# Performance work log

Hardware: AMD Instinct MI355X
Metric: run time of the kernel (lower is better)

Reference implementation:

```python
import jax, jax.numpy as jnp
import numpy as np

B = 256        # graphs per batch (python loop in original, vectorized here)
N = 512        # nodes per graph
DEG = 16       # avg degree
E_PER = N * DEG
T = 64         # num_node_types
D = 128        # gnn_hidden_dim


def setup_inputs() -> dict:
    key = jax.random.key(0)
    ks = jax.random.split(key, 8)
    node_feat = jax.random.randint(ks[0], (B * N,), 0, T)
    offs = (jnp.arange(B) * N)[:, None]
    src = (jax.random.randint(ks[1], (B, E_PER), 0, N) + offs).reshape(-1)
    dst = (jax.random.randint(ks[2], (B, E_PER), 0, N) + offs).reshape(-1)
    emb_table = jax.random.normal(ks[3], (T, D), dtype=jnp.float32) * 0.02
    W1 = jax.random.normal(ks[4], (D, D), dtype=jnp.float32) * (1.0 / np.sqrt(D))
    b1 = jnp.zeros((D,), dtype=jnp.float32)
    W2 = jax.random.normal(ks[5], (D, D), dtype=jnp.float32) * (1.0 / np.sqrt(D))
    b2 = jnp.zeros((D,), dtype=jnp.float32)
    return {"node_feat": node_feat, "src": src, "dst": dst,
            "emb_table": emb_table, "W1": W1, "b1": b1, "W2": W2, "b2": b2}


def _gcn_layer(h, src, dst, out_isqrt, in_isqrt, W, b, n):
    # DGL GraphConv, norm='both': D_in^{-1/2} A D_out^{-1/2} h W + b
    m = (h * out_isqrt[:, None])[src]                      # [E, D] gather
    agg = jax.ops.segment_sum(m, dst, num_segments=n)      # [Ntot, D] scatter
    return (agg * in_isqrt[:, None]) @ W + b


def reference(node_feat, src, dst, emb_table, W1, b1, W2, b2):
    n = node_feat.shape[0]
    ones = jnp.ones(src.shape[0], dtype=emb_table.dtype)
    deg_out = jnp.clip(jax.ops.segment_sum(ones, src, num_segments=n), 1.0)
    deg_in = jnp.clip(jax.ops.segment_sum(ones, dst, num_segments=n), 1.0)
    out_isqrt = jax.lax.rsqrt(deg_out)
    in_isqrt = jax.lax.rsqrt(deg_in)

    h = emb_table[node_feat]                                # [Ntot, D]
    # layer 1 (dropout is eval-mode identity) + relu, layer 2 + relu
    h = jax.nn.relu(_gcn_layer(h, src, dst, out_isqrt, in_isqrt, W1, b1, n))
    h = jax.nn.relu(_gcn_layer(h, src, dst, out_isqrt, in_isqrt, W2, b2, n))

    # dgl.mean_nodes per graph, then mean_gnn_embeddings + stack -> [B, D]
    gid = jnp.arange(n) // N
    hg = jax.ops.segment_sum(h, gid, num_segments=B) / float(N)
    return hg
```

## Files before the change

### kernel.cpp

```cpp
#include <hip/hip_runtime.h>
#include <stdint.h>

#define GRAPHS 256
#define NPG    512
#define EPG    8192

typedef __attribute__((ext_vector_type(8))) short s16x8;
typedef __attribute__((ext_vector_type(4))) float f32x4;

__device__ __forceinline__ float bf2f(unsigned short u){
  union { unsigned int i; float f; } c; c.i = ((unsigned int)u)<<16; return c.f;
}
__device__ __forceinline__ unsigned short f2bf(float f){
  union { float f; unsigned int i; } c; c.f = f;
  unsigned int r = c.i + 0x7fffu + ((c.i>>16)&1u);
  return (unsigned short)(r>>16);
}

__global__ __launch_bounds__(128) void k_prep(const float* __restrict__ emb,
      const float* __restrict__ W1, const float* __restrict__ W2,
      unsigned short* __restrict__ EW1T, unsigned short* __restrict__ W2F){
  const int b = blockIdx.x, tid = threadIdx.x;
  if (tid < 32){
    const int gid = b*32 + tid;
    const int t = gid>>7, c = gid&127;
    float acc=0.f;
    #pragma unroll 4
    for (int k=0;k<128;k++) acc += emb[t*128+k]*W1[k*128+c];
    EW1T[c*64+t]=f2bf(acc);
  } else if (tid >= 64){
    const int i = b*64 + (tid-64);
    const int ks = i>>12, nt=(i>>9)&7, ln=(i>>3)&63, j=i&7;
    const int k = ks*32 + (ln>>4)*8 + j;
    const int n = nt*16 + (ln&15);
    W2F[i] = f2bf(W2[k*128+n]);
  }
}

#define OFF_SORT 0
#define OFF_CS   16384
#define OFF_WSC  18440
#define OFF_WINT 20488
#define OFF_B1   22536
#define OFF_B2   23048
#define OFF_H1F  23568
#define OFF_SINT 89104
#define OFF_CSRA 23568
#define OFF_A    23568
#define OFF_ABF  40464
#define OFF_GBH  73744
#define OFF_GBL  82448
#define FUSED_LDS 158736

__global__ __launch_bounds__(512,2) void k_fused(
      const int* __restrict__ src, const int* __restrict__ dst,
      const int* __restrict__ ntype, const float* __restrict__ b1,
      const float* __restrict__ b2, const unsigned short* __restrict__ EW1T,
      const unsigned short* __restrict__ W2F, float* __restrict__ out){
  extern __shared__ char smem[];
  unsigned short* sorted16 = (unsigned short*)(smem + OFF_SORT);
  int*   cs   = (int*)(smem + OFF_CS);
  float* wsc  = (float*)(smem + OFF_WSC);
  int*   wint = (int*)(smem + OFF_WINT);
  float* b1sh = (float*)(smem + OFF_B1);
  float* b2sh = (float*)(smem + OFF_B2);
  unsigned short* h1F = (unsigned short*)(smem + OFF_H1F);
  int*   Sint = (int*)(smem + OFF_SINT);
  unsigned char*  A   = (unsigned char*)(smem + OFF_A);
  unsigned int*   A32 = (unsigned int*)(smem + OFF_A);
  unsigned short* Abf = (unsigned short*)(smem + OFF_ABF);
  unsigned short* gbh = (unsigned short*)(smem + OFF_GBH);
  unsigned short* gbl = (unsigned short*)(smem + OFF_GBL);
  float* red = (float*)(smem + OFF_A);
  int* hist   = (int*)(smem + OFF_CSRA);
  int* cursor = hist + 512;
  int* co     = cursor + 512;
  unsigned short* ntype_sh = (unsigned short*)(co + 512);

  const int b = blockIdx.x, tid = threadIdx.x;
  const int eb = b*EPG, nb = b*NPG;

  hist[tid]=0; co[tid]=0; ntype_sh[tid]=(unsigned short)ntype[nb+tid];
  if (tid<128){ b1sh[tid]=b1[tid]; b2sh[tid]=b2[tid]; }
  __syncthreads();
  int4 d4[4], s4[4];
  {
    const int4* dv = (const int4*)(dst+eb);
    const int4* sv = (const int4*)(src+eb);
    #pragma unroll
    for (int j=0;j<4;j++){
      d4[j]=dv[tid + j*512];
      s4[j]=sv[tid + j*512];
      atomicAdd(&hist[d4[j].x&(NPG-1)],1); atomicAdd(&hist[d4[j].y&(NPG-1)],1);
      atomicAdd(&hist[d4[j].z&(NPG-1)],1); atomicAdd(&hist[d4[j].w&(NPG-1)],1);
      atomicAdd(&co[s4[j].x&(NPG-1)],1);   atomicAdd(&co[s4[j].y&(NPG-1)],1);
      atomicAdd(&co[s4[j].z&(NPG-1)],1);   atomicAdd(&co[s4[j].w&(NPG-1)],1);
    }
  }
  __syncthreads();
  if (tid<64){
    int carry=0;
    #pragma unroll
    for (int c=0;c<8;c++){
      int sc=hist[64*c+tid];
      #pragma unroll
      for (int off=1;off<64;off<<=1){ int y=__shfl_up(sc,off); if (tid>=off) sc+=y; }
      cs[64*c+tid+1]=carry+sc;
      carry+=__shfl(sc,63);
    }
    if (tid==0) cs[0]=0;
  }
  __syncthreads();
  cursor[tid]=cs[tid];
  __syncthreads();
  #pragma unroll
  for (int j=0;j<4;j++){
    int dl, s, pos;
    dl=d4[j].x&(NPG-1); s=s4[j].x&(NPG-1);
    pos=atomicAdd(&cursor[dl],1);
    sorted16[pos]=(unsigned short)(((unsigned int)ntype_sh[s]<<9)|(unsigned int)s);
    dl=d4[j].y&(NPG-1); s=s4[j].y&(NPG-1);
    pos=atomicAdd(&cursor[dl],1);
    sorted16[pos]=(unsigned short)(((unsigned int)ntype_sh[s]<<9)|(unsigned int)s);
    dl=d4[j].z&(NPG-1); s=s4[j].z&(NPG-1);
    pos=atomicAdd(&cursor[dl],1);
    sorted16[pos]=(unsigned short)(((unsigned int)ntype_sh[s]<<9)|(unsigned int)s);
    dl=d4[j].w&(NPG-1); s=s4[j].w&(NPG-1);
    pos=atomicAdd(&cursor[dl],1);
    sorted16[pos]=(unsigned short)(((unsigned int)ntype_sh[s]<<9)|(unsigned int)s);
  }
  {
    int a=co[tid]; if(a<1)a=1;
    const float w = rsqrtf((float)a);
    wsc[tid]=w; wint[tid]=(int)(w*1048576.f);
  }
  __syncthreads();

  const int wave=tid>>6, lane=tid&63, l16=lane&15, quad=lane>>4;

  #pragma unroll 1
  for (int h=0; h<2; ++h){
    const int v0 = h*256;
    for (int i=tid; i<(256*68)/4; i+=512) ((f32x4*)Sint)[i]=(f32x4){0.f,0.f,0.f,0.f};
    __syncthreads();
    {
      const int r = tid>>1, p = tid&1;
      const int e1 = cs[v0+r+1];
      for (int i=cs[v0+r]+p; i<e1; i+=2){
        const unsigned int e = sorted16[i];
        atomicAdd(&Sint[r*68 + (int)(e>>9)], wint[e&511]);
      }
    }
    __syncthreads();
    f32x4 acc1[2][8];
    #pragma unroll
    for (int rt=0;rt<2;rt++)
      #pragma unroll
      for (int nt=0;nt<8;nt++) acc1[rt][nt]=(f32x4){0.f,0.f,0.f,0.f};
    #pragma unroll
    for (int kh=0; kh<2; ++kh){
      s16x8 fh[2], fl[2];
      #pragma unroll
      for (int rt=0;rt<2;rt++){
        const int m = (wave*2+rt)*16 + l16;
        const int* sp = &Sint[m*68 + kh*32 + quad*8];
        union { s16x8 v; unsigned short u[8]; } hv, lv;
        #pragma unroll
        for (int j=0;j<8;j++){
          const float f = (float)sp[j] * (1.f/1048576.f);
          const unsigned short hi = f2bf(f);
          hv.u[j]=hi; lv.u[j]=f2bf(f - bf2f(hi));
        }
        fh[rt]=hv.v; fl[rt]=lv.v;
      }
      const int kc = kh*32 + quad*8;
      #pragma unroll
      for (int nt=0;nt<8;nt++){
        s16x8 bfr=__builtin_bit_cast(s16x8,
            *(const uint4*)(EW1T + (size_t)(nt*16+l16)*64 + kc));
        acc1[0][nt]=__builtin_amdgcn_mfma_f32_16x16x32_bf16(fh[0],bfr,acc1[0][nt],0,0,0);
        acc1[1][nt]=__builtin_amdgcn_mfma_f32_16x16x32_bf16(fh[1],bfr,acc1[1][nt],0,0,0);
        acc1[0][nt]=__builtin_amdgcn_mfma_f32_16x16x32_bf16(fl[0],bfr,acc1[0][nt],0,0,0);
        acc1[1][nt]=__builtin_amdgcn_mfma_f32_16x16x32_bf16(fl[1],bfr,acc1[1][nt],0,0,0);
      }
    }
    float isq[2][4], os[2][4];
    #pragma unroll
    for (int rt=0;rt<2;rt++){
      const int mloc = (wave*2+rt)*16 + quad*4;
      #pragma unroll
      for (int r=0;r<4;r++){
        int d = cs[v0+mloc+r+1]-cs[v0+mloc+r]; if (d<1) d=1;
        isq[rt][r]=rsqrtf((float)d);
        os[rt][r]=wsc[v0+mloc+r];
      }
    }
    __syncthreads();
    #pragma unroll
    for (int rt=0;rt<2;rt++){
      const int ksg = h*8 + wave;
      const int kq  = rt*2 + (quad>>1);
      const int j0  = (quad&1)*4;
      #pragma unroll
      for (int nt=0;nt<8;nt++){
        const int col = nt*16+l16;
        const float bb1 = b1sh[col];
        ushort4 st;
        st.x = f2bf(fmaxf(acc1[rt][nt][0]*isq[rt][0]+bb1,0.f)*os[rt][0]);
        st.y = f2bf(fmaxf(acc1[rt][nt][1]*isq[rt][1]+bb1,0.f)*os[rt][1]);
        st.z = f2bf(fmaxf(acc1[rt][nt][2]*isq[rt][2]+bb1,0.f)*os[rt][2]);
        st.w = f2bf(fmaxf(acc1[rt][nt][3]*isq[rt][3]+bb1,0.f)*os[rt][3]);
        *(ushort4*)(h1F + ((((ksg*8+nt)*64) + kq*16 + l16)*8 + j0)) = st;
      }
    }
    __syncthreads();
  }

  s16x8 bh[16];
  #pragma unroll
  for (int ks=0;ks<16;ks++)
    bh[ks] = __builtin_bit_cast(s16x8,
        *(const uint4*)(h1F + (((ks*8+wave)*64 + lane)*8)));
  uint4 w2q[4];
  #pragma unroll
  for (int ks2=0;ks2<4;ks2++)
    w2q[ks2] = *(const uint4*)(W2F + (size_t)(((ks2*8+wave)*64)+lane)*8);
  const float bb2 = b2sh[wave*16+l16];
  __syncthreads();
  for (int i=tid; i<16896/16; i+=512) ((uint4*)A)[i]=(uint4){0u,0u,0u,0u};
  __syncthreads();
  float pp = 0.f;
  const int crow = tid>>4, ccol = (tid&15)*32;

  #pragma unroll 1
  for (int dt=0; dt<16; ++dt){
    const int r0 = dt*32;
    {
      const int r = tid>>4, p = tid&15;
      const int e1 = cs[r0+r+1];
      for (int i=cs[r0+r]+p; i<e1; i+=16){
        const int s = (int)(sorted16[i] & 511u);
        atomicAdd(&A32[r*132 + (s>>2)], 1u<<((s&3)*8));
      }
    }
    __syncthreads();
    {
      unsigned char* ap = A + crow*528 + ccol;
      const uint4 w0c = *(const uint4*)ap;
      const uint4 w1c = *(const uint4*)(ap+16);
      *(uint4*)ap = (uint4){0u,0u,0u,0u};
      *(uint4*)(ap+16) = (uint4){0u,0u,0u,0u};
      unsigned int wd[8] = {w0c.x,w0c.y,w0c.z,w0c.w,w1c.x,w1c.y,w1c.z,w1c.w};
      const int gb = (ccol>>3), sw = crow&7;
      #pragma unroll
      for (int ch=0; ch<4; ++ch){
        uint4 st;
        unsigned int u0=wd[2*ch], u1=wd[2*ch+1];
        {
          const float g0=(float)( u0       &0xffu);
          const float g1=(float)((u0>> 8u) &0xffu);
          const float g2=(float)((u0>>16u) &0xffu);
          const float g3=(float)( u0>>24u        );
          st.x=__builtin_amdgcn_perm(__builtin_bit_cast(unsigned int,g1),
                                     __builtin_bit_cast(unsigned int,g0),0x07060302u);
          st.y=__builtin_amdgcn_perm(__builtin_bit_cast(unsigned int,g3),
                                     __builtin_bit_cast(unsigned int,g2),0x07060302u);
        }
        {
          const float g0=(float)( u1       &0xffu);
          const float g1=(float)((u1>> 8u) &0xffu);
          const float g2=(float)((u1>>16u) &0xffu);
          const float g3=(float)( u1>>24u        );
          st.z=__builtin_amdgcn_perm(__builtin_bit_cast(unsigned int,g1),
                                     __builtin_bit_cast(unsigned int,g0),0x07060302u);
          st.w=__builtin_amdgcn_perm(__builtin_bit_cast(unsigned int,g3),
                                     __builtin_bit_cast(unsigned int,g2),0x07060302u);
        }
        *(uint4*)(Abf + crow*520 + (((gb+ch)^sw)<<3)) = st;
      }
    }
    __syncthreads();
    f32x4 g0=(f32x4){0.f,0.f,0.f,0.f}, g1=(f32x4){0.f,0.f,0.f,0.f};
    #pragma unroll
    for (int ks=0;ks<16;ks++){
      const int gsw = ((ks*4+quad) ^ (l16&7))<<3;
      const s16x8 a0 = __builtin_bit_cast(s16x8,
          *(const uint4*)(Abf + ( 0+l16)*520 + gsw));
      const s16x8 a1 = __builtin_bit_cast(s16x8,
          *(const uint4*)(Abf + (16+l16)*520 + gsw));
      g0=__builtin_amdgcn_mfma_f32_16x16x32_bf16(a0, bh[ks], g0,0,0,0);
      g1=__builtin_amdgcn_mfma_f32_16x16x32_bf16(a1, bh[ks], g1,0,0,0);
    }
    #pragma unroll
    for (int ri=0;ri<4;ri++){
      {
        const int row = quad*4+ri;
        int d = cs[r0+row+1]-cs[r0+row]; if (d<1) d=1;
        const float gs = g0[ri]*rsqrtf((float)d);
        const unsigned short hi = f2bf(gs);
        gbh[row*136 + wave*16+l16] = hi;
        gbl[row*136 + wave*16+l16] = f2bf(gs - bf2f(hi));
      }
      {
        const int row = 16+quad*4+ri;
        int d = cs[r0+row+1]-cs[r0+row]; if (d<1) d=1;
        const float gs = g1[ri]*rsqrtf((float)d);
        const unsigned short hi = f2bf(gs);
        gbh[row*136 + wave*16+l16] = hi;
        gbl[row*136 + wave*16+l16] = f2bf(gs - bf2f(hi));
      }
    }
    __syncthreads();
    f32x4 h30=(f32x4){0.f,0.f,0.f,0.f}, h31=(f32x4){0.f,0.f,0.f,0.f};
    #pragma unroll
    for (int ks2=0;ks2<4;ks2++){
      const int ko = ks2*32 + quad*8;
      h30=__builtin_amdgcn_mfma_f32_16x16x32_bf16(__builtin_bit_cast(s16x8,
          *(const uint4*)(gbh + ( 0+l16)*136 + ko)),
          __builtin_bit_cast(s16x8,w2q[ks2]), h30,0,0,0);
      h30=__builtin_amdgcn_mfma_f32_16x16x32_bf16(__builtin_bit_cast(s16x8,
          *(const uint4*)(gbl + ( 0+l16)*136 + ko)),
          __builtin_bit_cast(s16x8,w2q[ks2]), h30,0,0,0);
      h31=__builtin_amdgcn_mfma_f32_16x16x32_bf16(__builtin_bit_cast(s16x8,
          *(const uint4*)(gbh + (16+l16)*136 + ko)),
          __builtin_bit_cast(s16x8,w2q[ks2]), h31,0,0,0);
      h31=__builtin_amdgcn_mfma_f32_16x16x32_bf16(__builtin_bit_cast(s16x8,
          *(const uint4*)(gbl + (16+l16)*136 + ko)),
          __builtin_bit_cast(s16x8,w2q[ks2]), h31,0,0,0);
    }
    #pragma unroll
    for (int ri=0;ri<4;ri++){
      pp += fmaxf(h30[ri]+bb2, 0.f);
      pp += fmaxf(h31[ri]+bb2, 0.f);
    }
  }

  pp += __shfl_xor(pp,16);
  pp += __shfl_xor(pp,32);
  __syncthreads();
  if (quad==0) red[wave*16+l16] = pp;
  __syncthreads();
  if (tid<128) out[(size_t)b*128 + tid] = red[tid]*(1.f/512.f);
}

extern "C" void kernel_launch(void* const* d_in, const int* in_sizes, int n_in,
                              void* d_out, int out_size, void* d_ws, size_t ws_size,
                              hipStream_t stream){
  const int* node_feat = (const int*)d_in[0];
  const int* src = (const int*)d_in[1];
  const int* dst = (const int*)d_in[2];
  const float* emb = (const float*)d_in[3];
  const float* W1  = (const float*)d_in[4];
  const float* b1  = (const float*)d_in[5];
  const float* W2  = (const float*)d_in[6];
  const float* b2  = (const float*)d_in[7];

  char* ws = (char*)d_ws;
  unsigned short* EW1T = (unsigned short*)(ws);
  unsigned short* W2F  = (unsigned short*)(ws + 16384);

  (void)hipFuncSetAttribute(reinterpret_cast<const void*>(&k_fused),
        hipFuncAttributeMaxDynamicSharedMemorySize, FUSED_LDS);

  k_prep<<<GRAPHS,128,0,stream>>>(emb,W1,W2,EW1T,W2F);
  k_fused<<<GRAPHS,512,FUSED_LDS,stream>>>(src,dst,node_feat,b1,b2,EW1T,W2F,
        (float*)d_out);
}
```

Baseline: 166.4 us.

## Double threads per graph block to 1024 and split MFMA tiles across 16 waves

The fused per-graph kernel moves from 512 to 1024 threads per block. Edge loading, the weighted scatter, and the adjacency build are spread over more threads, and each of the 16 waves now computes one 16-row MFMA tile instead of two, with a final reduction over the two row halves. The prep kernel is also regridded to 64 blocks of 512 threads, and the layer-1 dot product is split over two lanes joined with a shuffle. This raises parallelism inside each block but drops the XOR swizzle on the Abf LDS layout, which may add bank conflicts. It also goes from two resident blocks per CU to one at 1024 threads, with more barrier cost per block.

Result: faster. 149.7 us (-10.1%).

```diff
diff --git a/kernel.cpp b/kernel.cpp
--- a/kernel.cpp
+++ b/kernel.cpp
@@ -17,19 +17,21 @@
   return (unsigned short)(r>>16);
 }
 
-__global__ __launch_bounds__(128) void k_prep(const float* __restrict__ emb,
+__global__ __launch_bounds__(512) void k_prep(const float* __restrict__ emb,
       const float* __restrict__ W1, const float* __restrict__ W2,
       unsigned short* __restrict__ EW1T, unsigned short* __restrict__ W2F){
-  const int b = blockIdx.x, tid = threadIdx.x;
-  if (tid < 32){
-    const int gid = b*32 + tid;
+  const int bid = blockIdx.x, tid = threadIdx.x;
+  if (bid < 32){
+    const int gid = bid*256 + (tid>>1);
+    const int p = tid&1;
     const int t = gid>>7, c = gid&127;
     float acc=0.f;
-    #pragma unroll 4
-    for (int k=0;k<128;k++) acc += emb[t*128+k]*W1[k*128+c];
-    EW1T[c*64+t]=f2bf(acc);
-  } else if (tid >= 64){
-    const int i = b*64 + (tid-64);
+    #pragma unroll 8
+    for (int k=p*64;k<p*64+64;k++) acc += emb[t*128+k]*W1[k*128+c];
+    const float other = __shfl_xor(acc,1);
+    if (p==0) EW1T[c*64+t]=f2bf(acc+other);
+  } else {
+    const int i = (bid-32)*512 + tid;
     const int ks = i>>12, nt=(i>>9)&7, ln=(i>>3)&63, j=i&7;
     const int k = ks*32 + (ln>>4)*8 + j;
     const int n = nt*16 + (ln&15);
@@ -52,7 +54,7 @@
 #define OFF_GBL  82448
 #define FUSED_LDS 158736
 
-__global__ __launch_bounds__(512,2) void k_fused(
+__global__ __launch_bounds__(1024,1) void k_fused(
       const int* __restrict__ src, const int* __restrict__ dst,
       const int* __restrict__ ntype, const float* __restrict__ b1,
       const float* __restrict__ b2, const unsigned short* __restrict__ EW1T,
@@ -80,17 +82,18 @@
   const int b = blockIdx.x, tid = threadIdx.x;
   const int eb = b*EPG, nb = b*NPG;
 
-  hist[tid]=0; co[tid]=0; ntype_sh[tid]=(unsigned short)ntype[nb+tid];
+  if (tid<512){ hist[tid]=0; co[tid]=0;
+                ntype_sh[tid]=(unsigned short)ntype[nb+tid]; }
   if (tid<128){ b1sh[tid]=b1[tid]; b2sh[tid]=b2[tid]; }
   __syncthreads();
-  int4 d4[4], s4[4];
+  int4 d4[2], s4[2];
   {
     const int4* dv = (const int4*)(dst+eb);
     const int4* sv = (const int4*)(src+eb);
     #pragma unroll
-    for (int j=0;j<4;j++){
-      d4[j]=dv[tid + j*512];
-      s4[j]=sv[tid + j*512];
+    for (int j=0;j<2;j++){
+      d4[j]=dv[tid + j*1024];
+      s4[j]=sv[tid + j*1024];
       atomicAdd(&hist[d4[j].x&(NPG-1)],1); atomicAdd(&hist[d4[j].y&(NPG-1)],1);
       atomicAdd(&hist[d4[j].z&(NPG-1)],1); atomicAdd(&hist[d4[j].w&(NPG-1)],1);
       atomicAdd(&co[s4[j].x&(NPG-1)],1);   atomicAdd(&co[s4[j].y&(NPG-1)],1);
@@ -111,10 +114,10 @@
     if (tid==0) cs[0]=0;
   }
   __syncthreads();
-  cursor[tid]=cs[tid];
+  if (tid<512) cursor[tid]=cs[tid];
   __syncthreads();
   #pragma unroll
-  for (int j=0;j<4;j++){
+  for (int j=0;j<2;j++){
     int dl, s, pos;
     dl=d4[j].x&(NPG-1); s=s4[j].x&(NPG-1);
     pos=atomicAdd(&cursor[dl],1);
@@ -129,7 +132,7 @@
     pos=atomicAdd(&cursor[dl],1);
     sorted16[pos]=(unsigned short)(((unsigned int)ntype_sh[s]<<9)|(unsigned int)s);
   }
-  {
+  if (tid<512){
     int a=co[tid]; if(a<1)a=1;
     const float w = rsqrtf((float)a);
     wsc[tid]=w; wint[tid]=(int)(w*1048576.f);
@@ -141,28 +144,25 @@
   #pragma unroll 1
   for (int h=0; h<2; ++h){
     const int v0 = h*256;
-    for (int i=tid; i<(256*68)/4; i+=512) ((f32x4*)Sint)[i]=(f32x4){0.f,0.f,0.f,0.f};
-    __syncthreads();
-    {
-      const int r = tid>>1, p = tid&1;
+    for (int i=tid; i<(256*68)/4; i+=1024) ((f32x4*)Sint)[i]=(f32x4){0.f,0.f,0.f,0.f};
+    __syncthreads();
+    {
+      const int r = tid>>2, p = tid&3;
       const int e1 = cs[v0+r+1];
-      for (int i=cs[v0+r]+p; i<e1; i+=2){
+      for (int i=cs[v0+r]+p; i<e1; i+=4){
         const unsigned int e = sorted16[i];
         atomicAdd(&Sint[r*68 + (int)(e>>9)], wint[e&511]);
       }
     }
     __syncthreads();
-    f32x4 acc1[2][8];
-    #pragma unroll
-    for (int rt=0;rt<2;rt++)
-      #pragma unroll
-      for (int nt=0;nt<8;nt++) acc1[rt][nt]=(f32x4){0.f,0.f,0.f,0.f};
+    f32x4 acc1[8];
+    #pragma unroll
+    for (int nt=0;nt<8;nt++) acc1[nt]=(f32x4){0.f,0.f,0.f,0.f};
     #pragma unroll
     for (int kh=0; kh<2; ++kh){
-      s16x8 fh[2], fl[2];
-      #pragma unroll
-      for (int rt=0;rt<2;rt++){
-        const int m = (wave*2+rt)*16 + l16;
+      s16x8 fh, fl;
+      {
+        const int m = wave*16 + l16;
         const int* sp = &Sint[m*68 + kh*32 + quad*8];
         union { s16x8 v; unsigned short u[8]; } hv, lv;
         #pragma unroll
@@ -171,45 +171,41 @@
           const unsigned short hi = f2bf(f);
           hv.u[j]=hi; lv.u[j]=f2bf(f - bf2f(hi));
         }
-        fh[rt]=hv.v; fl[rt]=lv.v;
+        fh=hv.v; fl=lv.v;
       }
       const int kc = kh*32 + quad*8;
       #pragma unroll
       for (int nt=0;nt<8;nt++){
         s16x8 bfr=__builtin_bit_cast(s16x8,
             *(const uint4*)(EW1T + (size_t)(nt*16+l16)*64 + kc));
-        acc1[0][nt]=__builtin_amdgcn_mfma_f32_16x16x32_bf16(fh[0],bfr,acc1[0][nt],0,0,0);
-        acc1[1][nt]=__builtin_amdgcn_mfma_f32_16x16x32_bf16(fh[1],bfr,acc1[1][nt],0,0,0);
-        acc1[0][nt]=__builtin_amdgcn_mfma_f32_16x16x32_bf16(fl[0],bfr,acc1[0][nt],0,0,0);
-        acc1[1][nt]=__builtin_amdgcn_mfma_f32_16x16x32_bf16(fl[1],bfr,acc1[1][nt],0,0,0);
-      }
-    }
-    float isq[2][4], os[2][4];
-    #pragma unroll
-    for (int rt=0;rt<2;rt++){
-      const int mloc = (wave*2+rt)*16 + quad*4;
+        acc1[nt]=__builtin_amdgcn_mfma_f32_16x16x32_bf16(fh,bfr,acc1[nt],0,0,0);
+        acc1[nt]=__builtin_amdgcn_mfma_f32_16x16x32_bf16(fl,bfr,acc1[nt],0,0,0);
+      }
+    }
+    float isq[4], os[4];
+    {
+      const int mloc = wave*16 + quad*4;
       #pragma unroll
       for (int r=0;r<4;r++){
         int d = cs[v0+mloc+r+1]-cs[v0+mloc+r]; if (d<1) d=1;
-        isq[rt][r]=rsqrtf((float)d);
-        os[rt][r]=wsc[v0+mloc+r];
-      }
-    }
-    __syncthreads();
-    #pragma unroll
-    for (int rt=0;rt<2;rt++){
-      const int ksg = h*8 + wave;
-      const int kq  = rt*2 + (quad>>1);
+        isq[r]=rsqrtf((float)d);
+        os[r]=wsc[v0+mloc+r];
+      }
+    }
+    __syncthreads();
+    {
+      const int ksg = h*8 + (wave>>1);
+      const int kq  = (wave&1)*2 + (quad>>1);
       const int j0  = (quad&1)*4;
       #pragma unroll
       for (int nt=0;nt<8;nt++){
         const int col = nt*16+l16;
         const float bb1 = b1sh[col];
         ushort4 st;
-        st.x = f2bf(fmaxf(acc1[rt][nt][0]*isq[rt][0]+bb1,0.f)*os[rt][0]);
-        st.y = f2bf(fmaxf(acc1[rt][nt][1]*isq[rt][1]+bb1,0.f)*os[rt][1]);
-        st.z = f2bf(fmaxf(acc1[rt][nt][2]*isq[rt][2]+bb1,0.f)*os[rt][2]);
-        st.w = f2bf(fmaxf(acc1[rt][nt][3]*isq[rt][3]+bb1,0.f)*os[rt][3]);
+        st.x = f2bf(fmaxf(acc1[nt][0]*isq[0]+bb1,0.f)*os[0]);
+        st.y = f2bf(fmaxf(acc1[nt][1]*isq[1]+bb1,0.f)*os[1]);
+        st.z = f2bf(fmaxf(acc1[nt][2]*isq[2]+bb1,0.f)*os[2]);
+        st.w = f2bf(fmaxf(acc1[nt][3]*isq[3]+bb1,0.f)*os[3]);
         *(ushort4*)(h1F + ((((ksg*8+nt)*64) + kq*16 + l16)*8 + j0)) = st;
       }
     }
@@ -220,25 +216,26 @@
   #pragma unroll
   for (int ks=0;ks<16;ks++)
     bh[ks] = __builtin_bit_cast(s16x8,
-        *(const uint4*)(h1F + (((ks*8+wave)*64 + lane)*8)));
+        *(const uint4*)(h1F + (((ks*8+(wave&7))*64 + lane)*8)));
   uint4 w2q[4];
   #pragma unroll
   for (int ks2=0;ks2<4;ks2++)
-    w2q[ks2] = *(const uint4*)(W2F + (size_t)(((ks2*8+wave)*64)+lane)*8);
-  const float bb2 = b2sh[wave*16+l16];
-  __syncthreads();
-  for (int i=tid; i<16896/16; i+=512) ((uint4*)A)[i]=(uint4){0u,0u,0u,0u};
+    w2q[ks2] = *(const uint4*)(W2F + (size_t)(((ks2*8+(wave&7))*64)+lane)*8);
+  const float bb2 = b2sh[(wave&7)*16+l16];
+  const int mt = wave>>3, ntw = wave&7;
+  __syncthreads();
+  for (int i=tid; i<16896/16; i+=1024) ((uint4*)A)[i]=(uint4){0u,0u,0u,0u};
   __syncthreads();
   float pp = 0.f;
-  const int crow = tid>>4, ccol = (tid&15)*32;
+  const int crow = tid&31, ccol = (tid>>5)*16;
 
   #pragma unroll 1
   for (int dt=0; dt<16; ++dt){
     const int r0 = dt*32;
     {
-      const int r = tid>>4, p = tid&15;
+      const int r = tid>>5, p = tid&31;
       const int e1 = cs[r0+r+1];
-      for (int i=cs[r0+r]+p; i<e1; i+=16){
+      for (int i=cs[r0+r]+p; i<e1; i+=32){
         const int s = (int)(sorted16[i] & 511u);
         atomicAdd(&A32[r*132 + (s>>2)], 1u<<((s&3)*8));
       }
@@ -247,92 +244,83 @@
     {
       unsigned char* ap = A + crow*528 + ccol;
       const uint4 w0c = *(const uint4*)ap;
-      const uint4 w1c = *(const uint4*)(ap+16);
       *(uint4*)ap = (uint4){0u,0u,0u,0u};
-      *(uint4*)(ap+16) = (uint4){0u,0u,0u,0u};
-      unsigned int wd[8] = {w0c.x,w0c.y,w0c.z,w0c.w,w1c.x,w1c.y,w1c.z,w1c.w};
-      const int gb = (ccol>>3), sw = crow&7;
-      #pragma unroll
-      for (int ch=0; ch<4; ++ch){
-        uint4 st;
-        unsigned int u0=wd[2*ch], u1=wd[2*ch+1];
-        {
-          const float g0=(float)( u0       &0xffu);
-          const float g1=(float)((u0>> 8u) &0xffu);
-          const float g2=(float)((u0>>16u) &0xffu);
-          const float g3=(float)( u0>>24u        );
-          st.x=__builtin_amdgcn_perm(__builtin_bit_cast(unsigned int,g1),
-                                     __builtin_bit_cast(unsigned int,g0),0x07060302u);
-          st.y=__builtin_amdgcn_perm(__builtin_bit_cast(unsigned int,g3),
-                                     __builtin_bit_cast(unsigned int,g2),0x07060302u);
-        }
-        {
-          const float g0=(float)( u1       &0xffu);
-          const float g1=(float)((u1>> 8u) &0xffu);
-          const float g2=(float)((u1>>16u) &0xffu);
-          const float g3=(float)( u1>>24u        );
-          st.z=__builtin_amdgcn_perm(__builtin_bit_cast(unsigned int,g1),
-                                     __builtin_bit_cast(unsigned int,g0),0x07060302u);
-          st.w=__builtin_amdgcn_perm(__builtin_bit_cast(unsigned int,g3),
-                                     __builtin_bit_cast(unsigned int,g2),0x07060302u);
-        }
-        *(uint4*)(Abf + crow*520 + (((gb+ch)^sw)<<3)) = st;
-      }
-    }
-    __syncthreads();
-    f32x4 g0=(f32x4){0.f,0.f,0.f,0.f}, g1=(f32x4){0.f,0.f,0.f,0.f};
+      const int g0i = ccol>>3;
+      uint4 st0, st1;
+      {
+        const float g0=(float)( w0c.x       &0xffu);
+        const float g1=(float)((w0c.x>> 8u) &0xffu);
+        const float g2=(float)((w0c.x>>16u) &0xffu);
+        const float g3=(float)( w0c.x>>24u        );
+        st0.x=__builtin_amdgcn_perm(__builtin_bit_cast(unsigned int,g1),
+                                    __builtin_bit_cast(unsigned int,g0),0x07060302u);
+        st0.y=__builtin_amdgcn_perm(__builtin_bit_cast(unsigned int,g3),
+                                    __builtin_bit_cast(unsigned int,g2),0x07060302u);
+      }
+      {
+        const float g0=(float)( w0c.y       &0xffu);
+        const float g1=(float)((w0c.y>> 8u) &0xffu);
+        const float g2=(float)((w0c.y>>16u) &0xffu);
+        const float g3=(float)( w0c.y>>24u        );
+        st0.z=__builtin_amdgcn_perm(__builtin_bit_cast(unsigned int,g1),
+                                    __builtin_bit_cast(unsigned int,g0),0x07060302u);
+        st0.w=__builtin_amdgcn_perm(__builtin_bit_cast(unsigned int,g3),
+                                    __builtin_bit_cast(unsigned int,g2),0x07060302u);
+      }
+      {
+        const float g0=(float)( w0c.z       &0xffu);
+        const float g1=(float)((w0c.z>> 8u) &0xffu);
+        const float g2=(float)((w0c.z>>16u) &0xffu);
+        const float g3=(float)( w0c.z>>24u        );
+        st1.x=__builtin_amdgcn_perm(__builtin_bit_cast(unsigned int,g1),
+                                    __builtin_bit_cast(unsigned int,g0),0x07060302u);
+        st1.y=__builtin_amdgcn_perm(__builtin_bit_cast(unsigned int,g3),
+                                    __builtin_bit_cast(unsigned int,g2),0x07060302u);
+      }
+      {
+        const float g0=(float)( w0c.w       &0xffu);
+        const float g1=(float)((w0c.w>> 8u) &0xffu);
+        const float g2=(float)((w0c.w>>16u) &0xffu);
+        const float g3=(float)( w0c.w>>24u        );
+        st1.z=__builtin_amdgcn_perm(__builtin_bit_cast(unsigned int,g1),
+                                    __builtin_bit_cast(unsigned int,g0),0x07060302u);
+        st1.w=__builtin_amdgcn_perm(__builtin_bit_cast(unsigned int,g3),
+                                    __builtin_bit_cast(unsigned int,g2),0x07060302u);
+      }
+      *(uint4*)(Abf + crow*520 + ((g0i  )<<3)) = st0;
+      *(uint4*)(Abf + crow*520 + ((g0i+1)<<3)) = st1;
+    }
+    __syncthreads();
+    f32x4 g0v=(f32x4){0.f,0.f,0.f,0.f};
     #pragma unroll
     for (int ks=0;ks<16;ks++){
-      const int gsw = ((ks*4+quad) ^ (l16&7))<<3;
       const s16x8 a0 = __builtin_bit_cast(s16x8,
-          *(const uint4*)(Abf + ( 0+l16)*520 + gsw));
-      const s16x8 a1 = __builtin_bit_cast(s16x8,
-          *(const uint4*)(Abf + (16+l16)*520 + gsw));
-      g0=__builtin_amdgcn_mfma_f32_16x16x32_bf16(a0, bh[ks], g0,0,0,0);
-      g1=__builtin_amdgcn_mfma_f32_16x16x32_bf16(a1, bh[ks], g1,0,0,0);
+          *(const uint4*)(Abf + (mt*16+l16)*520 + ((ks*4+quad)<<3)));
+      g0v=__builtin_amdgcn_mfma_f32_16x16x32_bf16(a0, bh[ks], g0v,0,0,0);
     }
     #pragma unroll
     for (int ri=0;ri<4;ri++){
-      {
-        const int row = quad*4+ri;
-        int d = cs[r0+row+1]-cs[r0+row]; if (d<1) d=1;
-        const float gs = g0[ri]*rsqrtf((float)d);
-        const unsigned short hi = f2bf(gs);
-        gbh[row*136 + wave*16+l16] = hi;
-        gbl[row*136 + wave*16+l16] = f2bf(gs - bf2f(hi));
-      }
-      {
-        const int row = 16+quad*4+ri;
-        int d = cs[r0+row+1]-cs[r0+row]; if (d<1) d=1;
-        const float gs = g1[ri]*rsqrtf((float)d);
-        const unsigned short hi = f2bf(gs);
-        gbh[row*136 + wave*16+l16] = hi;
-        gbl[row*136 + wave*16+l16] = f2bf(gs - bf2f(hi));
-      }
-    }
-    __syncthreads();
-    f32x4 h30=(f32x4){0.f,0.f,0.f,0.f}, h31=(f32x4){0.f,0.f,0.f,0.f};
+      const int row = mt*16 + quad*4+ri;
+      int d = cs[r0+row+1]-cs[r0+row]; if (d<1) d=1;
+      const float gs = g0v[ri]*rsqrtf((float)d);
+      const unsigned short hi = f2bf(gs);
+      gbh[row*136 + ntw*16+l16] = hi;
+      gbl[row*136 + ntw*16+l16] = f2bf(gs - bf2f(hi));
+    }
+    __syncthreads();
+    f32x4 h30=(f32x4){0.f,0.f,0.f,0.f};
     #pragma unroll
     for (int ks2=0;ks2<4;ks2++){
       const int ko = ks2*32 + quad*8;
       h30=__builtin_amdgcn_mfma_f32_16x16x32_bf16(__builtin_bit_cast(s16x8,
-          *(const uint4*)(gbh + ( 0+l16)*136 + ko)),
+          *(const uint4*)(gbh + (mt*16+l16)*136 + ko)),
           __builtin_bit_cast(s16x8,w2q[ks2]), h30,0,0,0);
       h30=__builtin_amdgcn_mfma_f32_16x16x32_bf16(__builtin_bit_cast(s16x8,
-          *(const uint4*)(gbl + ( 0+l16)*136 + ko)),
+          *(const uint4*)(gbl + (mt*16+l16)*136 + ko)),
           __builtin_bit_cast(s16x8,w2q[ks2]), h30,0,0,0);
-      h31=__builtin_amdgcn_mfma_f32_16x16x32_bf16(__builtin_bit_cast(s16x8,
-          *(const uint4*)(gbh + (16+l16)*136 + ko)),
-          __builtin_bit_cast(s16x8,w2q[ks2]), h31,0,0,0);
-      h31=__builtin_amdgcn_mfma_f32_16x16x32_bf16(__builtin_bit_cast(s16x8,
-          *(const uint4*)(gbl + (16+l16)*136 + ko)),
-          __builtin_bit_cast(s16x8,w2q[ks2]), h31,0,0,0);
-    }
-    #pragma unroll
-    for (int ri=0;ri<4;ri++){
-      pp += fmaxf(h30[ri]+bb2, 0.f);
-      pp += fmaxf(h31[ri]+bb2, 0.f);
-    }
+    }
+    #pragma unroll
+    for (int ri=0;ri<4;ri++) pp += fmaxf(h30[ri]+bb2, 0.f);
   }
 
   pp += __shfl_xor(pp,16);
@@ -340,7 +328,7 @@
   __syncthreads();
   if (quad==0) red[wave*16+l16] = pp;
   __syncthreads();
-  if (tid<128) out[(size_t)b*128 + tid] = red[tid]*(1.f/512.f);
+  if (tid<128) out[(size_t)b*128 + tid] = (red[tid]+red[128+tid])*(1.f/512.f);
 }
 
 extern "C" void kernel_launch(void* const* d_in, const int* in_sizes, int n_in,
@@ -362,7 +350,7 @@
   (void)hipFuncSetAttribute(reinterpret_cast<const void*>(&k_fused),
         hipFuncAttributeMaxDynamicSharedMemorySize, FUSED_LDS);
 
-  k_prep<<<GRAPHS,128,0,stream>>>(emb,W1,W2,EW1T,W2F);
-  k_fused<<<GRAPHS,512,FUSED_LDS,stream>>>(src,dst,node_feat,b1,b2,EW1T,W2F,
+  k_prep<<<64,512,0,stream>>>(emb,W1,W2,EW1T,W2F);
+  k_fused<<<GRAPHS,1024,FUSED_LDS,stream>>>(src,dst,node_feat,b1,b2,EW1T,W2F,
         (float*)d_out);
 }
```
